# Performance work log

Measured on AMD Instinct MI355X. Metric: run time of the kernel, lower is better.

## Reference

```python
import jax, jax.numpy as jnp
import numpy as np

N_NODES = 100000
N_EDGES = 1600000
IN_CH = 165


def setup_inputs() -> dict:
    key = jax.random.key(0)
    ks = jax.random.split(key, 6)
    x = jax.random.normal(ks[0], (N_NODES, IN_CH), dtype=jnp.float32)
    edge_index = jax.random.randint(ks[1], (2, N_EDGES), 0, N_NODES, dtype=jnp.int32)
    # Glorot-ish init for weights
    W1 = jax.random.normal(ks[2], (IN_CH, 128), dtype=jnp.float32) * (1.0 / np.sqrt(IN_CH))
    b1 = jnp.zeros((128,), dtype=jnp.float32)
    W2 = jax.random.normal(ks[3], (128, 64), dtype=jnp.float32) * (1.0 / np.sqrt(128))
    b2 = jnp.zeros((64,), dtype=jnp.float32)
    Wo = jax.random.normal(ks[4], (64, 2), dtype=jnp.float32) * (1.0 / np.sqrt(64))
    bo = jnp.zeros((2,), dtype=jnp.float32)
    return {"x": x, "edge_index": edge_index, "W1": W1, "b1": b1,
            "W2": W2, "b2": b2, "Wo": Wo, "bo": bo}


def _gcn_norm(edge_index, n_nodes, dtype):
    """Add self-loops and compute symmetric normalization deg^-1/2 * deg^-1/2 (PyG gcn_norm)."""
    loops = jnp.arange(n_nodes, dtype=edge_index.dtype)
    ei = jnp.concatenate([edge_index, jnp.stack([loops, loops])], axis=1)
    row, col = ei[0], ei[1]
    deg = jax.ops.segment_sum(jnp.ones(ei.shape[1], dtype), col, num_segments=n_nodes)
    deg_inv_sqrt = jnp.where(deg > 0, jax.lax.rsqrt(deg), 0.0)
    norm = deg_inv_sqrt[row] * deg_inv_sqrt[col]  # [E+N]
    return row, col, norm


def _gcn_conv(h, row, col, norm, W, b, n_nodes):
    # transform first (F_in -> F_out), then gather-scale-scatter aggregate
    m = h @ W                                   # [N, F_out]
    msg = m[row] * norm[:, None]                # [E+N, F_out]
    agg = jax.ops.segment_sum(msg, col, num_segments=n_nodes)
    return agg + b


def reference(x, edge_index, W1, b1, W2, b2, Wo, bo):
    n_nodes = x.shape[0]
    row, col, norm = _gcn_norm(edge_index, n_nodes, x.dtype)
    h = jax.nn.relu(_gcn_conv(x, row, col, norm, W1, b1, n_nodes))
    h = jax.nn.relu(_gcn_conv(h, row, col, norm, W2, b2, n_nodes))
    return h @ Wo + bo  # [N, 2] logits
```

## Files before the change

kernel.cpp:

```cpp
#include <hip/hip_runtime.h>

#define N_NODES 100000
#define N_EDGES 1600000
#define IN_CH   165
#define SCAN_CHUNK 2048
#define NB_SCAN ((N_NODES + SCAN_CHUNK - 1) / SCAN_CHUNK)
#define BSHIFT 7
#define NBUCK  ((N_NODES + 127) / 128)
#define BCAP   3072
#define PA_BLOCKS 196

typedef unsigned short ushort_t;
typedef _Float16 f16;
typedef _Float16 f16x2 __attribute__((ext_vector_type(2)));
typedef short bfrag8 __attribute__((ext_vector_type(8)));
typedef float f32x4 __attribute__((ext_vector_type(4)));

__device__ __forceinline__ ushort_t f2bf(float f) {
    unsigned u = __float_as_uint(f);
    unsigned r = (u + 0x7fffu + ((u >> 16) & 1u)) >> 16;
    return (ushort_t)r;
}
__device__ __forceinline__ float bf2f(ushort_t h) {
    return __uint_as_float(((unsigned)h) << 16);
}

__global__ void scan1_kernel(const int* __restrict__ cnt, int* __restrict__ off,
                             int* __restrict__ bsum, int n) {
    __shared__ int sh[256];
    int t = threadIdx.x;
    int base = blockIdx.x * SCAN_CHUNK + t * 8;
    int v[8];
    int run = 0;
    #pragma unroll
    for (int j = 0; j < 8; ++j) {
        int c = (base + j < n) ? cnt[base + j] : 0;
        v[j] = run; run += c;
    }
    sh[t] = run;
    __syncthreads();
    for (int o = 1; o < 256; o <<= 1) {
        int x = (t >= o) ? sh[t - o] : 0;
        __syncthreads();
        sh[t] += x;
        __syncthreads();
    }
    int prev = (t > 0) ? sh[t - 1] : 0;
    #pragma unroll
    for (int j = 0; j < 8; ++j)
        if (base + j < n) off[base + j] = prev + v[j];
    if (t == 255) bsum[blockIdx.x] = sh[255];
}

__global__ void scan2_kernel(int* bsum, int nb) {
    int lane = threadIdx.x;
    int orig = (lane < nb) ? bsum[lane] : 0;
    int v = orig;
    #pragma unroll
    for (int o = 1; o < 64; o <<= 1) {
        int t = __shfl_up(v, o);
        if (lane >= o) v += t;
    }
    if (lane < nb) bsum[lane] = v - orig;
}

__global__ void scan3_kernel(int* __restrict__ off, const int* __restrict__ bsum,
                             int n, int E) {
    int i = blockIdx.x * blockDim.x + threadIdx.x;
    if (i < n) {
        off[i] = off[i] + bsum[i / SCAN_CHUNK];
    } else if (i == n) {
        off[n] = E;
    }
}

__global__ void bucketA_kernel(const int* __restrict__ row, const int* __restrict__ col,
                               int* __restrict__ bfill, unsigned* __restrict__ tmp) {
    __shared__ int lcnt[NBUCK];
    __shared__ int lcur[NBUCK];
    int t = threadIdx.x;
    int e0 = (int)((long)blockIdx.x * N_EDGES / PA_BLOCKS);
    int e1 = (int)((long)(blockIdx.x + 1) * N_EDGES / PA_BLOCKS);
    for (int i = t; i < NBUCK; i += 256) lcnt[i] = 0;
    __syncthreads();
    for (int e = e0 + t; e < e1; e += 256)
        atomicAdd(&lcnt[col[e] >> BSHIFT], 1);
    __syncthreads();
    for (int b = t; b < NBUCK; b += 256) {
        int c = lcnt[b];
        lcur[b] = (c > 0) ? (b * BCAP + atomicAdd(&bfill[b], c)) : 0;
    }
    __syncthreads();
    for (int e = e0 + t; e < e1; e += 256) {
        int cc = col[e];
        int b = cc >> BSHIFT;
        int p = atomicAdd(&lcur[b], 1);
        tmp[p] = ((unsigned)(cc & 127) << 17) | (unsigned)row[e];
    }
}

__global__ void countB_kernel(const unsigned* __restrict__ tmp, const int* __restrict__ bfill,
                              int* __restrict__ cnt, float* __restrict__ dis) {
    __shared__ int lcnt[128];
    int b = blockIdx.x, t = threadIdx.x;
    if (t < 128) lcnt[t] = 0;
    __syncthreads();
    int total = min(bfill[b], BCAP);
    const unsigned* reg = tmp + (size_t)b * BCAP;
    for (int i = t; i < total; i += 256)
        atomicAdd(&lcnt[(reg[i] >> 17) & 127], 1);
    __syncthreads();
    if (t < 128) {
        int n = (b << BSHIFT) + t;
        if (n < N_NODES) {
            int c = lcnt[t];
            cnt[n] = c;
            dis[n] = rsqrtf((float)(c + 1));
        }
    }
}

__global__ void bucketB_kernel(const unsigned* __restrict__ tmp, const int* __restrict__ bfill,
                               const int* __restrict__ off, int* __restrict__ srt) {
    __shared__ int lcur[128];
    int b = blockIdx.x;
    int t = threadIdx.x;
    int nb0 = b << BSHIFT;
    int hi = min(nb0 + 128, N_NODES);
    int base = off[nb0];
    if (t < 128) {
        int nn = nb0 + t;
        lcur[t] = (nn < hi) ? off[nn] - base : 0;
    }
    __syncthreads();
    int total = min(bfill[b], BCAP);
    const unsigned* reg = tmp + (size_t)b * BCAP;
    for (int i = t; i < total; i += 256) {
        unsigned e = reg[i];
        int c = (e >> 17) & 127;
        int r = (int)(e & 0x1FFFFu);
        int p = atomicAdd(&lcur[c], 1);
        srt[base + p] = r;
    }
}

__global__ void wsplit_kernel(const float* __restrict__ W1, const float* __restrict__ W2,
                              ushort_t* __restrict__ wt1h, ushort_t* __restrict__ wt1l,
                              ushort_t* __restrict__ wt2h, ushort_t* __restrict__ wt2l) {
    int i = blockIdx.x * 256 + threadIdx.x;
    if (i < 128 * 192) {
        int ch = i / 192, k = i - ch * 192;
        float v = (k < IN_CH) ? W1[(size_t)k * 128 + ch] : 0.f;
        ushort_t h = f2bf(v);
        wt1h[i] = h;
        wt1l[i] = f2bf(v - bf2f(h));
    } else if (i < 128 * 192 + 64 * 128) {
        int j = i - 128 * 192;
        int ch = j / 128, k = j - ch * 128;
        float v = W2[(size_t)k * 64 + ch];
        ushort_t h = f2bf(v);
        wt2h[j] = h;
        wt2l[j] = f2bf(v - bf2f(h));
    }
}

template<int NOUT, int KTOT, int KPAD>
__launch_bounds__(256)
__global__ void mfma_gemm_kernel(const float* __restrict__ X,
                                 const ushort_t* __restrict__ wth,
                                 const ushort_t* __restrict__ wtl,
                                 const float* __restrict__ dis,
                                 f16* __restrict__ M, int n_nodes) {
    constexpr int NCT = NOUT / 16;
    constexpr int NCHUNK = KPAD / 32;
    constexpr int XP = 40;
    constexpr int NW = (NOUT * 4 + 255) / 256;
    __shared__ ushort_t xsh[64][XP];
    __shared__ ushort_t xsl[64][XP];
    __shared__ ushort_t wsh[NOUT][XP];
    __shared__ ushort_t wsl[NOUT][XP];

    int t = threadIdx.x;
    int l = t & 63, wid = t >> 6;
    long node0 = (long)blockIdx.x * 64;

    int arow = wid * 16 + (l & 15);
    int kq = (l >> 4) * 8;

    f32x4 acc[NCT];
    #pragma unroll
    for (int ct = 0; ct < NCT; ++ct) acc[ct] = (f32x4){0.f, 0.f, 0.f, 0.f};

    float xa[4], xb[4];
    bfrag8 wfh[NW], wfl[NW];

    auto loadX = [&](int c) {
        int k0 = c * 32;
        #pragma unroll
        for (int i = 0; i < 4; ++i) {
            int idx = t + i * 256;
            int node = idx >> 4, kp = idx & 15;
            long g = node0 + node;
            int k = k0 + 2 * kp;
            bool ok = (g < n_nodes);
            xa[i] = (ok && k < KTOT) ? X[g * KTOT + k] : 0.f;
            xb[i] = (ok && k + 1 < KTOT) ? X[g * KTOT + k + 1] : 0.f;
        }
    };
    auto loadW = [&](int c) {
        int k0 = c * 32;
        #pragma unroll
        for (int i = 0; i < NW; ++i) {
            int idx = t + i * 256;
            int ch = idx >> 2, q = idx & 3;
            wfh[i] = *(const bfrag8*)&wth[(size_t)ch * KPAD + k0 + q * 8];
            wfl[i] = *(const bfrag8*)&wtl[(size_t)ch * KPAD + k0 + q * 8];
        }
    };
    auto storeLDS = [&]() {
        #pragma unroll
        for (int i = 0; i < 4; ++i) {
            int idx = t + i * 256;
            int node = idx >> 4, kp = idx & 15;
            ushort_t ha = (ushort_t)(__float_as_uint(xa[i]) >> 16);
            ushort_t la = f2bf(xa[i] - bf2f(ha));
            ushort_t hb = (ushort_t)(__float_as_uint(xb[i]) >> 16);
            ushort_t lb = f2bf(xb[i] - bf2f(hb));
            *(unsigned*)&xsh[node][2 * kp] = (unsigned)ha | ((unsigned)hb << 16);
            *(unsigned*)&xsl[node][2 * kp] = (unsigned)la | ((unsigned)lb << 16);
        }
        #pragma unroll
        for (int i = 0; i < NW; ++i) {
            int idx = t + i * 256;
            int ch = idx >> 2, q = idx & 3;
            *(bfrag8*)&wsh[ch][q * 8] = wfh[i];
            *(bfrag8*)&wsl[ch][q * 8] = wfl[i];
        }
    };

    loadX(0); loadW(0);
    for (int c = 0; c < NCHUNK; ++c) {
        storeLDS();
        __syncthreads();
        if (c + 1 < NCHUNK) { loadX(c + 1); loadW(c + 1); }
        bfrag8 ah = *(const bfrag8*)&xsh[arow][kq];
        bfrag8 al = *(const bfrag8*)&xsl[arow][kq];
        #pragma unroll
        for (int ct = 0; ct < NCT; ++ct) {
            bfrag8 bh = *(const bfrag8*)&wsh[ct * 16 + (l & 15)][kq];
            bfrag8 bl = *(const bfrag8*)&wsl[ct * 16 + (l & 15)][kq];
            acc[ct] = __builtin_amdgcn_mfma_f32_16x16x32_bf16(ah, bh, acc[ct], 0, 0, 0);
            acc[ct] = __builtin_amdgcn_mfma_f32_16x16x32_bf16(ah, bl, acc[ct], 0, 0, 0);
            acc[ct] = __builtin_amdgcn_mfma_f32_16x16x32_bf16(al, bh, acc[ct], 0, 0, 0);
        }
        __syncthreads();
    }

    int nl = wid * 16 + (l >> 4) * 4;
    float dv[4];
    #pragma unroll
    for (int j = 0; j < 4; ++j) {
        long node = node0 + nl + j;
        dv[j] = (node < n_nodes) ? dis[node] : 0.f;
    }
    #pragma unroll
    for (int ct = 0; ct < NCT; ++ct) {
        int ch = ct * 16 + (l & 15);
        #pragma unroll
        for (int j = 0; j < 4; ++j) {
            long node = node0 + nl + j;
            if (node < n_nodes)
                M[node * NOUT + ch] = (f16)(acc[ct][j] * dv[j]);
        }
    }
}

__global__ void agg1_kernel(const f16* __restrict__ ms, const int* __restrict__ srt,
                            const int* __restrict__ off, const float* __restrict__ dis,
                            const float* __restrict__ b1, float* __restrict__ h1) {
    int wave = threadIdx.x >> 6;
    int lane = threadIdx.x & 63;
    int n = blockIdx.x * 4 + wave;
    if (n >= N_NODES) return;
    float dn = dis[n];
    f16x2 a = ((const f16x2*)(ms + (size_t)n * 128))[lane];
    float accx = (float)a.x, accy = (float)a.y;
    int s0 = off[n], s1 = off[n + 1];
    int sv = (s0 + lane < s1) ? srt[s0 + lane] : 0;
    for (int base = s0; base < s1; base += 64) {
        int nb2 = base + 64;
        int svn = (nb2 + lane < s1) ? srt[nb2 + lane] : 0;
        int cnt = min(64, s1 - base);
        int j = 0;
        for (; j + 15 < cnt; j += 16) {
            f16x2 v[16];
            #pragma unroll
            for (int u = 0; u < 16; ++u)
                v[u] = ((const f16x2*)(ms + (size_t)__builtin_amdgcn_readlane(sv, j + u) * 128))[lane];
            #pragma unroll
            for (int u = 0; u < 16; ++u) { accx += (float)v[u].x; accy += (float)v[u].y; }
        }
        for (; j + 3 < cnt; j += 4) {
            f16x2 v[4];
            #pragma unroll
            for (int u = 0; u < 4; ++u)
                v[u] = ((const f16x2*)(ms + (size_t)__builtin_amdgcn_readlane(sv, j + u) * 128))[lane];
            #pragma unroll
            for (int u = 0; u < 4; ++u) { accx += (float)v[u].x; accy += (float)v[u].y; }
        }
        for (; j < cnt; ++j) {
            f16x2 v = ((const f16x2*)(ms + (size_t)__builtin_amdgcn_readlane(sv, j) * 128))[lane];
            accx += (float)v.x; accy += (float)v.y;
        }
        sv = svn;
    }
    float2 b = ((const float2*)b1)[lane];
    float rx = fmaxf(accx * dn + b.x, 0.f);
    float ry = fmaxf(accy * dn + b.y, 0.f);
    ((float2*)(h1 + (size_t)n * 128))[lane] = make_float2(rx, ry);
}

__global__ void agg2_kernel(const f16* __restrict__ ms, const int* __restrict__ srt,
                            const int* __restrict__ off, const float* __restrict__ dis,
                            const float* __restrict__ b2, const float* __restrict__ Wo,
                            const float* __restrict__ bo, float* __restrict__ out) {
    int wave = threadIdx.x >> 6;
    int lane = threadIdx.x & 63;
    int n = blockIdx.x * 4 + wave;
    if (n >= N_NODES) return;
    float dn = dis[n];
    float acc = (float)ms[(size_t)n * 64 + lane];
    int s0 = off[n], s1 = off[n + 1];
    int sv = (s0 + lane < s1) ? srt[s0 + lane] : 0;
    for (int base = s0; base < s1; base += 64) {
        int nb2 = base + 64;
        int svn = (nb2 + lane < s1) ? srt[nb2 + lane] : 0;
        int cnt = min(64, s1 - base);
        int j = 0;
        for (; j + 15 < cnt; j += 16) {
            f16 v[16];
            #pragma unroll
            for (int u = 0; u < 16; ++u)
                v[u] = ms[(size_t)__builtin_amdgcn_readlane(sv, j + u) * 64 + lane];
            #pragma unroll
            for (int u = 0; u < 16; ++u) acc += (float)v[u];
        }
        for (; j + 3 < cnt; j += 4) {
            f16 v[4];
            #pragma unroll
            for (int u = 0; u < 4; ++u)
                v[u] = ms[(size_t)__builtin_amdgcn_readlane(sv, j + u) * 64 + lane];
            #pragma unroll
            for (int u = 0; u < 4; ++u) acc += (float)v[u];
        }
        for (; j < cnt; ++j)
            acc += (float)ms[(size_t)__builtin_amdgcn_readlane(sv, j) * 64 + lane];
        sv = svn;
    }
    float v = fmaxf(acc * dn + b2[lane], 0.f);
    float p0 = v * Wo[lane * 2];
    float p1 = v * Wo[lane * 2 + 1];
    #pragma unroll
    for (int o = 32; o > 0; o >>= 1) {
        p0 += __shfl_xor(p0, o);
        p1 += __shfl_xor(p1, o);
    }
    if (lane == 0) {
        out[(size_t)n * 2]     = p0 + bo[0];
        out[(size_t)n * 2 + 1] = p1 + bo[1];
    }
}

extern "C" void kernel_launch(void* const* d_in, const int* in_sizes, int n_in,
                              void* d_out, int out_size, void* d_ws, size_t ws_size,
                              hipStream_t stream) {
    const float* x  = (const float*)d_in[0];
    const int*   ei = (const int*)d_in[1];
    const int*   row = ei;
    const int*   col = ei + N_EDGES;
    const float* W1 = (const float*)d_in[2];
    const float* b1 = (const float*)d_in[3];
    const float* W2 = (const float*)d_in[4];
    const float* b2 = (const float*)d_in[5];
    const float* Wo = (const float*)d_in[6];
    const float* bo = (const float*)d_in[7];
    float* out = (float*)d_out;

    char* base = (char*)d_ws;
    auto alloc = [&](size_t bytes) {
        char* p = base;
        base += (bytes + 255) & ~(size_t)255;
        return p;
    };
    int*      cnt  = (int*)alloc((size_t)N_NODES * 4);
    int*      off  = (int*)alloc((size_t)(N_NODES + 1) * 4);
    float*    dis  = (float*)alloc((size_t)N_NODES * 4);
    int*      bsum = (int*)alloc(256);
    int*      bfill= (int*)alloc((size_t)NBUCK * 4);
    unsigned* tmp  = (unsigned*)alloc((size_t)NBUCK * BCAP * 4 + 4096);
    int*      srt  = (int*)alloc((size_t)N_EDGES * 4);
    f16*      m    = (f16*)alloc((size_t)N_NODES * 128 * 2);
    float*    h1   = (float*)alloc((size_t)N_NODES * 128 * 4);
    ushort_t* wt1h = (ushort_t*)alloc((size_t)128 * 192 * 2);
    ushort_t* wt1l = (ushort_t*)alloc((size_t)128 * 192 * 2);
    ushort_t* wt2h = (ushort_t*)alloc((size_t)64 * 128 * 2);
    ushort_t* wt2l = (ushort_t*)alloc((size_t)64 * 128 * 2);

    hipMemsetAsync(bfill, 0, (size_t)NBUCK * 4, stream);
    bucketA_kernel<<<PA_BLOCKS, 256, 0, stream>>>(row, col, bfill, tmp);
    countB_kernel<<<NBUCK, 256, 0, stream>>>(tmp, bfill, cnt, dis);
    scan1_kernel<<<NB_SCAN, 256, 0, stream>>>(cnt, off, bsum, N_NODES);
    scan2_kernel<<<1, 64, 0, stream>>>(bsum, NB_SCAN);
    scan3_kernel<<<(N_NODES + 256) / 256, 256, 0, stream>>>(off, bsum, N_NODES, N_EDGES);
    bucketB_kernel<<<NBUCK, 256, 0, stream>>>(tmp, bfill, off, srt);
    wsplit_kernel<<<(128 * 192 + 64 * 128 + 255) / 256, 256, 0, stream>>>(W1, W2, wt1h, wt1l, wt2h, wt2l);

    mfma_gemm_kernel<128, 165, 192><<<(N_NODES + 63) / 64, 256, 0, stream>>>(x, wt1h, wt1l, dis, m, N_NODES);
    agg1_kernel<<<(N_NODES + 3) / 4, 256, 0, stream>>>(m, srt, off, dis, b1, h1);

    mfma_gemm_kernel<64, 128, 128><<<(N_NODES + 63) / 64, 256, 0, stream>>>(h1, wt2h, wt2l, dis, m, N_NODES);
    agg2_kernel<<<(N_NODES + 3) / 4, 256, 0, stream>>>(m, srt, off, dis, b2, Wo, bo, out);
}
```

Measured before the change: 240.3 us.

## Vectorize neighbor gathers to 16-byte loads and store hidden layer in fp16

The aggregation kernels now have each lane load eight fp16 channels with one 16-byte load, so several neighbors are fetched per wave instruction. Partial sums are then combined with cross-lane shuffles. The intermediate h1 is stored as fp16 instead of fp32, which halves its write and its re-read by the second GEMM. In exchange this adds shuffle reductions and some precision loss in h1, and drops the prefetch of the next index chunk.

Result: no change. 238.9 us (-0.6%).

```diff
diff --git a/kernel.cpp b/kernel.cpp
--- a/kernel.cpp
+++ b/kernel.cpp
@@ -13,6 +13,7 @@
 typedef unsigned short ushort_t;
 typedef _Float16 f16;
 typedef _Float16 f16x2 __attribute__((ext_vector_type(2)));
+typedef _Float16 f16x8 __attribute__((ext_vector_type(8)));
 typedef short bfrag8 __attribute__((ext_vector_type(8)));
 typedef float f32x4 __attribute__((ext_vector_type(4)));
 
@@ -164,9 +165,9 @@
     }
 }
 
-template<int NOUT, int KTOT, int KPAD>
+template<int NOUT, int KTOT, int KPAD, bool F16IN>
 __launch_bounds__(256)
-__global__ void mfma_gemm_kernel(const float* __restrict__ X,
+__global__ void mfma_gemm_kernel(const void* __restrict__ Xv,
                                  const ushort_t* __restrict__ wth,
                                  const ushort_t* __restrict__ wtl,
                                  const float* __restrict__ dis,
@@ -203,8 +204,15 @@
             long g = node0 + node;
             int k = k0 + 2 * kp;
             bool ok = (g < n_nodes);
-            xa[i] = (ok && k < KTOT) ? X[g * KTOT + k] : 0.f;
-            xb[i] = (ok && k + 1 < KTOT) ? X[g * KTOT + k + 1] : 0.f;
+            if constexpr (F16IN) {
+                const f16* X = (const f16*)Xv;
+                xa[i] = (ok && k < KTOT) ? (float)X[g * KTOT + k] : 0.f;
+                xb[i] = (ok && k + 1 < KTOT) ? (float)X[g * KTOT + k + 1] : 0.f;
+            } else {
+                const float* X = (const float*)Xv;
+                xa[i] = (ok && k < KTOT) ? X[g * KTOT + k] : 0.f;
+                xb[i] = (ok && k + 1 < KTOT) ? X[g * KTOT + k + 1] : 0.f;
+            }
         }
     };
     auto loadW = [&](int c) {
@@ -277,47 +285,61 @@
 
 __global__ void agg1_kernel(const f16* __restrict__ ms, const int* __restrict__ srt,
                             const int* __restrict__ off, const float* __restrict__ dis,
-                            const float* __restrict__ b1, float* __restrict__ h1) {
+                            const float* __restrict__ b1, f16* __restrict__ h1) {
     int wave = threadIdx.x >> 6;
     int lane = threadIdx.x & 63;
     int n = blockIdx.x * 4 + wave;
     if (n >= N_NODES) return;
+    int g = lane >> 4, p = lane & 15;
     float dn = dis[n];
-    f16x2 a = ((const f16x2*)(ms + (size_t)n * 128))[lane];
-    float accx = (float)a.x, accy = (float)a.y;
+    float acc[8];
+    {
+        f16x8 v = *(const f16x8*)(ms + (size_t)n * 128 + p * 8);
+        float wm = (g == 0) ? 1.f : 0.f;
+        #pragma unroll
+        for (int i = 0; i < 8; ++i) acc[i] = wm * (float)v[i];
+    }
     int s0 = off[n], s1 = off[n + 1];
-    int sv = (s0 + lane < s1) ? srt[s0 + lane] : 0;
     for (int base = s0; base < s1; base += 64) {
-        int nb2 = base + 64;
-        int svn = (nb2 + lane < s1) ? srt[nb2 + lane] : 0;
+        int sv = (base + lane < s1) ? srt[base + lane] : 0;
         int cnt = min(64, s1 - base);
         int j = 0;
         for (; j + 15 < cnt; j += 16) {
-            f16x2 v[16];
+            int i0 = __shfl(sv, j + g);
+            int i1 = __shfl(sv, j + 4 + g);
+            int i2 = __shfl(sv, j + 8 + g);
+            int i3 = __shfl(sv, j + 12 + g);
+            f16x8 v0 = *(const f16x8*)(ms + (size_t)i0 * 128 + p * 8);
+            f16x8 v1 = *(const f16x8*)(ms + (size_t)i1 * 128 + p * 8);
+            f16x8 v2 = *(const f16x8*)(ms + (size_t)i2 * 128 + p * 8);
+            f16x8 v3 = *(const f16x8*)(ms + (size_t)i3 * 128 + p * 8);
             #pragma unroll
-            for (int u = 0; u < 16; ++u)
-                v[u] = ((const f16x2*)(ms + (size_t)__builtin_amdgcn_readlane(sv, j + u) * 128))[lane];
+            for (int i = 0; i < 8; ++i)
+                acc[i] += (float)v0[i] + (float)v1[i] + (float)v2[i] + (float)v3[i];
+        }
+        for (; j < cnt; j += 4) {
+            int idx = __shfl(sv, j + g);
+            float wm = (j + g < cnt) ? 1.f : 0.f;
+            f16x8 v = *(const f16x8*)(ms + (size_t)idx * 128 + p * 8);
             #pragma unroll
-            for (int u = 0; u < 16; ++u) { accx += (float)v[u].x; accy += (float)v[u].y; }
-        }
-        for (; j + 3 < cnt; j += 4) {
-            f16x2 v[4];
-            #pragma unroll
-            for (int u = 0; u < 4; ++u)
-                v[u] = ((const f16x2*)(ms + (size_t)__builtin_amdgcn_readlane(sv, j + u) * 128))[lane];
-            #pragma unroll
-            for (int u = 0; u < 4; ++u) { accx += (float)v[u].x; accy += (float)v[u].y; }
-        }
-        for (; j < cnt; ++j) {
-            f16x2 v = ((const f16x2*)(ms + (size_t)__builtin_amdgcn_readlane(sv, j) * 128))[lane];
-            accx += (float)v.x; accy += (float)v.y;
-        }
-        sv = svn;
-    }
-    float2 b = ((const float2*)b1)[lane];
-    float rx = fmaxf(accx * dn + b.x, 0.f);
-    float ry = fmaxf(accy * dn + b.y, 0.f);
-    ((float2*)(h1 + (size_t)n * 128))[lane] = make_float2(rx, ry);
+            for (int i = 0; i < 8; ++i) acc[i] = fmaf(wm, (float)v[i], acc[i]);
+        }
+    }
+    #pragma unroll
+    for (int i = 0; i < 8; ++i) {
+        acc[i] += __shfl_xor(acc[i], 16);
+        acc[i] += __shfl_xor(acc[i], 32);
+    }
+    if (lane < 16) {
+        float4 ba = ((const float4*)b1)[lane * 2];
+        float4 bb = ((const float4*)b1)[lane * 2 + 1];
+        float bv[8] = {ba.x, ba.y, ba.z, ba.w, bb.x, bb.y, bb.z, bb.w};
+        f16x8 r;
+        #pragma unroll
+        for (int i = 0; i < 8; ++i)
+            r[i] = (f16)fmaxf(acc[i] * dn + bv[i], 0.f);
+        *(f16x8*)(h1 + (size_t)n * 128 + lane * 8) = r;
+    }
 }
 
 __global__ void agg2_kernel(const f16* __restrict__ ms, const int* __restrict__ srt,
@@ -328,43 +350,54 @@
     int lane = threadIdx.x & 63;
     int n = blockIdx.x * 4 + wave;
     if (n >= N_NODES) return;
+    int g = lane >> 3, p = lane & 7;
     float dn = dis[n];
-    float acc = (float)ms[(size_t)n * 64 + lane];
+    float acc[8];
+    {
+        f16x8 v = *(const f16x8*)(ms + (size_t)n * 64 + p * 8);
+        float wm = (g == 0) ? 1.f : 0.f;
+        #pragma unroll
+        for (int i = 0; i < 8; ++i) acc[i] = wm * (float)v[i];
+    }
     int s0 = off[n], s1 = off[n + 1];
-    int sv = (s0 + lane < s1) ? srt[s0 + lane] : 0;
     for (int base = s0; base < s1; base += 64) {
-        int nb2 = base + 64;
-        int svn = (nb2 + lane < s1) ? srt[nb2 + lane] : 0;
+        int sv = (base + lane < s1) ? srt[base + lane] : 0;
         int cnt = min(64, s1 - base);
         int j = 0;
         for (; j + 15 < cnt; j += 16) {
-            f16 v[16];
+            int i0 = __shfl(sv, j + g);
+            int i1 = __shfl(sv, j + 8 + g);
+            f16x8 v0 = *(const f16x8*)(ms + (size_t)i0 * 64 + p * 8);
+            f16x8 v1 = *(const f16x8*)(ms + (size_t)i1 * 64 + p * 8);
             #pragma unroll
-            for (int u = 0; u < 16; ++u)
-                v[u] = ms[(size_t)__builtin_amdgcn_readlane(sv, j + u) * 64 + lane];
+            for (int i = 0; i < 8; ++i)
+                acc[i] += (float)v0[i] + (float)v1[i];
+        }
+        for (; j < cnt; j += 8) {
+            int idx = __shfl(sv, j + g);
+            float wm = (j + g < cnt) ? 1.f : 0.f;
+            f16x8 v = *(const f16x8*)(ms + (size_t)idx * 64 + p * 8);
             #pragma unroll
-            for (int u = 0; u < 16; ++u) acc += (float)v[u];
-        }
-        for (; j + 3 < cnt; j += 4) {
-            f16 v[4];
-            #pragma unroll
-            for (int u = 0; u < 4; ++u)
-                v[u] = ms[(size_t)__builtin_amdgcn_readlane(sv, j + u) * 64 + lane];
-            #pragma unroll
-            for (int u = 0; u < 4; ++u) acc += (float)v[u];
-        }
-        for (; j < cnt; ++j)
-            acc += (float)ms[(size_t)__builtin_amdgcn_readlane(sv, j) * 64 + lane];
-        sv = svn;
-    }
-    float v = fmaxf(acc * dn + b2[lane], 0.f);
-    float p0 = v * Wo[lane * 2];
-    float p1 = v * Wo[lane * 2 + 1];
-    #pragma unroll
-    for (int o = 32; o > 0; o >>= 1) {
-        p0 += __shfl_xor(p0, o);
-        p1 += __shfl_xor(p1, o);
-    }
+            for (int i = 0; i < 8; ++i) acc[i] = fmaf(wm, (float)v[i], acc[i]);
+        }
+    }
+    #pragma unroll
+    for (int i = 0; i < 8; ++i) {
+        acc[i] += __shfl_xor(acc[i], 8);
+        acc[i] += __shfl_xor(acc[i], 16);
+        acc[i] += __shfl_xor(acc[i], 32);
+    }
+    float p0 = 0.f, p1 = 0.f;
+    #pragma unroll
+    for (int i = 0; i < 8; ++i) {
+        int ch = p * 8 + i;
+        float hc = fmaxf(acc[i] * dn + b2[ch], 0.f);
+        p0 = fmaf(hc, Wo[ch * 2], p0);
+        p1 = fmaf(hc, Wo[ch * 2 + 1], p1);
+    }
+    p0 += __shfl_xor(p0, 1); p1 += __shfl_xor(p1, 1);
+    p0 += __shfl_xor(p0, 2); p1 += __shfl_xor(p1, 2);
+    p0 += __shfl_xor(p0, 4); p1 += __shfl_xor(p1, 4);
     if (lane == 0) {
         out[(size_t)n * 2]     = p0 + bo[0];
         out[(size_t)n * 2 + 1] = p1 + bo[1];
@@ -400,7 +433,7 @@
     unsigned* tmp  = (unsigned*)alloc((size_t)NBUCK * BCAP * 4 + 4096);
     int*      srt  = (int*)alloc((size_t)N_EDGES * 4);
     f16*      m    = (f16*)alloc((size_t)N_NODES * 128 * 2);
-    float*    h1   = (float*)alloc((size_t)N_NODES * 128 * 4);
+    f16*      h1   = (f16*)alloc((size_t)N_NODES * 128 * 2);
     ushort_t* wt1h = (ushort_t*)alloc((size_t)128 * 192 * 2);
     ushort_t* wt1l = (ushort_t*)alloc((size_t)128 * 192 * 2);
     ushort_t* wt2h = (ushort_t*)alloc((size_t)64 * 128 * 2);
@@ -415,9 +448,9 @@
     bucketB_kernel<<<NBUCK, 256, 0, stream>>>(tmp, bfill, off, srt);
     wsplit_kernel<<<(128 * 192 + 64 * 128 + 255) / 256, 256, 0, stream>>>(W1, W2, wt1h, wt1l, wt2h, wt2l);
 
-    mfma_gemm_kernel<128, 165, 192><<<(N_NODES + 63) / 64, 256, 0, stream>>>(x, wt1h, wt1l, dis, m, N_NODES);
+    mfma_gemm_kernel<128, 165, 192, false><<<(N_NODES + 63) / 64, 256, 0, stream>>>(x, wt1h, wt1l, dis, m, N_NODES);
     agg1_kernel<<<(N_NODES + 3) / 4, 256, 0, stream>>>(m, srt, off, dis, b1, h1);
 
-    mfma_gemm_kernel<64, 128, 128><<<(N_NODES + 63) / 64, 256, 0, stream>>>(h1, wt2h, wt2l, dis, m, N_NODES);
+    mfma_gemm_kernel<64, 128, 128, true><<<(N_NODES + 63) / 64, 256, 0, stream>>>(h1, wt2h, wt2l, dis, m, N_NODES);
     agg2_kernel<<<(N_NODES + 3) / 4, 256, 0, stream>>>(m, srt, off, dis, b2, Wo, bo, out);
 }
```
